# Performance work log

Hardware: AMD Instinct MI355X
Metric: run time of the kernel (lower is better)

The kernel has to match this reference:

```python
import jax, jax.numpy as jnp
import numpy as np

BSZ, IN_DIM, HID, OUT_DIM, N_ITERS = 262144, 64, 128, 64, 30


def setup_inputs() -> dict:
    key = jax.random.key(0)
    ks = jax.random.split(key, 6)
    s_h = 1.0 / np.sqrt(HID)
    s_i = 1.0 / np.sqrt(IN_DIM)
    return {
        "x": jax.random.normal(ks[0], (BSZ, IN_DIM), dtype=jnp.float32),
        "Wz": jax.random.uniform(ks[1], (HID, HID), jnp.float32, -s_h, s_h) * 0.9,  # scaled for contraction
        "Ux": jax.random.uniform(ks[2], (HID, IN_DIM), jnp.float32, -s_i, s_i),
        "b": jax.random.uniform(ks[3], (HID,), jnp.float32, -s_h, s_h),
        "Wd": jax.random.uniform(ks[4], (OUT_DIM, HID), jnp.float32, -s_h, s_h),
        "bd": jax.random.uniform(ks[5], (OUT_DIM,), jnp.float32, -s_h, s_h),
        "n_iters": N_ITERS,
    }


def reference(x, Wz, Ux, b, Wd, bd, n_iters):
    # injection term is iteration-invariant: compute once
    inj = x @ Ux.T + b                     # [B, HID]
    z0 = jnp.zeros((x.shape[0], Wz.shape[0]), dtype=x.dtype)

    def step(z, _):
        z = jax.nn.relu(z @ Wz.T + inj)    # f(z, x)
        return z, None

    z_star, _ = jax.lax.scan(step, z0, None, length=n_iters)
    return z_star @ Wd.T + bd              # decoder Linear
```

## Files before the change

### kernel.cpp

```cpp
#include <hip/hip_runtime.h>


typedef __attribute__((ext_vector_type(8))) __bf16 bf16x8;
typedef __attribute__((ext_vector_type(4))) __bf16 bf16x4;
typedef __attribute__((ext_vector_type(4))) float  floatx4;

#define MFMA16(a, b, c) __builtin_amdgcn_mfma_f32_16x16x32_bf16((a), (b), (c), 0, 0, 0)

static constexpr int kBsz = 262144;
static constexpr int kTM  = 32;

__device__ __forceinline__ bf16x8 cvt_bf16x8(float4 a, float4 b) {
  bf16x8 r;
  r[0] = (__bf16)a.x; r[1] = (__bf16)a.y; r[2] = (__bf16)a.z; r[3] = (__bf16)a.w;
  r[4] = (__bf16)b.x; r[5] = (__bf16)b.y; r[6] = (__bf16)b.z; r[7] = (__bf16)b.w;
  return r;
}

__global__ void __launch_bounds__(256, 4) deq_fused(
    const float* __restrict__ x,
    const float* __restrict__ Wz,
    const float* __restrict__ Ux,
    const float* __restrict__ bvec,
    const float* __restrict__ Wd,
    const float* __restrict__ bd,
    const int*  __restrict__ n_iters_p,
    float* __restrict__ out)
{
  __shared__ __align__(16) __bf16 zl[2][kTM][136];

  const int tid  = threadIdx.x;
  const int lane = tid & 63;
  const int wv   = tid >> 6;
  const int wn   = wv & 1;
  const int wm   = wv >> 1;
  const int l15  = lane & 15;
  const int quad = lane >> 4;
  const int row0 = blockIdx.x * kTM;
  const int ml   = 16 * wm + l15;
  const int iters = *n_iters_p;

  bf16x8 awz[4][4];
#pragma unroll
  for (int nt = 0; nt < 4; ++nt) {
    const int n = 64 * wn + 16 * nt + l15;
#pragma unroll
    for (int ks = 0; ks < 4; ++ks) {
      const float4* p = (const float4*)(Wz + n * 128 + 32 * ks + 8 * quad);
      awz[nt][ks] = cvt_bf16x8(p[0], p[1]);
    }
  }

  floatx4 inj[4];
#pragma unroll
  for (int nt = 0; nt < 4; ++nt) {
    const float4 bv = *(const float4*)(bvec + 64 * wn + 16 * nt + 4 * quad);
    floatx4 v = {bv.x, bv.y, bv.z, bv.w};
    inj[nt] = v;
  }
  {
    bf16x8 bx[2];
#pragma unroll
    for (int ks = 0; ks < 2; ++ks) {
      const float4* p = (const float4*)(x + (size_t)(row0 + ml) * 64 + 32 * ks + 8 * quad);
      bx[ks] = cvt_bf16x8(p[0], p[1]);
    }
#pragma unroll
    for (int nt = 0; nt < 4; ++nt) {
      const int n = 64 * wn + 16 * nt + l15;
#pragma unroll
      for (int ks = 0; ks < 2; ++ks) {
        const float4* p = (const float4*)(Ux + n * 64 + 32 * ks + 8 * quad);
        const bf16x8 a = cvt_bf16x8(p[0], p[1]);
        inj[nt] = MFMA16(a, bx[ks], inj[nt]);
      }
    }
  }

#pragma unroll
  for (int nt = 0; nt < 4; ++nt) {
    bf16x4 z4;
#pragma unroll
    for (int i = 0; i < 4; ++i) z4[i] = (__bf16)fmaxf(inj[nt][i], 0.0f);
    *(bf16x4*)&zl[0][ml][64 * wn + 16 * nt + 4 * quad] = z4;
  }

  int pb = 0;
  for (int t = 0; t < iters - 1; ++t) {
    __syncthreads();
    bf16x8 bz[4];
#pragma unroll
    for (int ks = 0; ks < 4; ++ks)
      bz[ks] = *(const bf16x8*)&zl[pb][ml][32 * ks + 8 * quad];
    const int nb = pb ^ 1;
#pragma unroll
    for (int nt = 0; nt < 4; ++nt) {
      floatx4 acc = inj[nt];
#pragma unroll
      for (int ks = 0; ks < 4; ++ks)
        acc = MFMA16(awz[nt][ks], bz[ks], acc);
      bf16x4 z4;
#pragma unroll
      for (int i = 0; i < 4; ++i) z4[i] = (__bf16)fmaxf(acc[i], 0.0f);
      *(bf16x4*)&zl[nb][ml][64 * wn + 16 * nt + 4 * quad] = z4;
    }
    pb = nb;
  }
  __syncthreads();

  bf16x8 awd[2][4];
#pragma unroll
  for (int ot = 0; ot < 2; ++ot) {
    const int o = 32 * wn + 16 * ot + l15;
#pragma unroll
    for (int ks = 0; ks < 4; ++ks) {
      const float4* p = (const float4*)(Wd + o * 128 + 32 * ks + 8 * quad);
      awd[ot][ks] = cvt_bf16x8(p[0], p[1]);
    }
  }
  {
    bf16x8 bz[4];
#pragma unroll
    for (int ks = 0; ks < 4; ++ks)
      bz[ks] = *(const bf16x8*)&zl[pb][ml][32 * ks + 8 * quad];
#pragma unroll
    for (int ot = 0; ot < 2; ++ot) {
      const float4 bv = *(const float4*)(bd + 32 * wn + 16 * ot + 4 * quad);
      floatx4 acc = {bv.x, bv.y, bv.z, bv.w};
#pragma unroll
      for (int ks = 0; ks < 4; ++ks)
        acc = MFMA16(awd[ot][ks], bz[ks], acc);
      float4 ov;
      ov.x = acc[0]; ov.y = acc[1]; ov.z = acc[2]; ov.w = acc[3];
      *(float4*)(out + (size_t)(row0 + ml) * 64 + 32 * wn + 16 * ot + 4 * quad) = ov;
    }
  }
}

extern "C" void kernel_launch(void* const* d_in, const int* in_sizes, int n_in,
                              void* d_out, int out_size, void* d_ws, size_t ws_size,
                              hipStream_t stream) {
  const float* x  = (const float*)d_in[0];
  const float* Wz = (const float*)d_in[1];
  const float* Ux = (const float*)d_in[2];
  const float* b  = (const float*)d_in[3];
  const float* Wd = (const float*)d_in[4];
  const float* bd = (const float*)d_in[5];
  const int* n_it = (const int*)d_in[6];
  float* outp = (float*)d_out;
  (void)in_sizes; (void)n_in; (void)d_ws; (void)ws_size; (void)out_size;

  dim3 grid(kBsz / kTM);
  deq_fused<<<grid, 256, 0, stream>>>(x, Wz, Ux, b, Wd, bd, n_it, outp);
}
```

Baseline: 378.9 us.

## Split decoder into separate kernel, staging bf16 fixed point in output buffer

Splits the fused kernel in two. The iteration kernel now writes the final bf16 z tile into the output buffer as scratch, and a second kernel reads it back, applies the Wd decoder with MFMA and overwrites the same rows with fp32 results. The intent is to free the decoder weight registers and code from the long iteration loop, which may lower register pressure or raise occupancy. In exchange it adds a second launch and roughly 128 MB of extra global memory traffic, and it relies on each row being read before it is overwritten in place.

```diff
diff --git a/kernel.cpp b/kernel.cpp
--- a/kernel.cpp
+++ b/kernel.cpp
@@ -9,6 +9,7 @@
 
 static constexpr int kBsz = 262144;
 static constexpr int kTM  = 32;
+static constexpr int kLd  = 136;
 
 __device__ __forceinline__ bf16x8 cvt_bf16x8(float4 a, float4 b) {
   bf16x8 r;
@@ -17,17 +18,15 @@
   return r;
 }
 
-__global__ void __launch_bounds__(256, 4) deq_fused(
+__global__ void __launch_bounds__(256, 4) deq_loop(
     const float* __restrict__ x,
     const float* __restrict__ Wz,
     const float* __restrict__ Ux,
     const float* __restrict__ bvec,
-    const float* __restrict__ Wd,
-    const float* __restrict__ bd,
     const int*  __restrict__ n_iters_p,
-    float* __restrict__ out)
+    __bf16* __restrict__ zout)
 {
-  __shared__ __align__(16) __bf16 zl[2][kTM][136];
+  __shared__ __align__(16) __bf16 zl[2][kTM][kLd];
 
   const int tid  = threadIdx.x;
   const int lane = tid & 63;
@@ -108,32 +107,46 @@
   }
   __syncthreads();
 
-  bf16x8 awd[2][4];
+  const int r = tid >> 3;
+  const int c = (tid & 7) * 16;
+  const bf16x8 zlo = *(const bf16x8*)&zl[pb][r][c];
+  const bf16x8 zhi = *(const bf16x8*)&zl[pb][r][c + 8];
+  *(bf16x8*)&zout[(size_t)(row0 + r) * 128 + c] = zlo;
+  *(bf16x8*)&zout[(size_t)(row0 + r) * 128 + c + 8] = zhi;
+}
+
+__global__ void __launch_bounds__(256) deq_dec(
+    const float* __restrict__ Wd,
+    const float* __restrict__ bd,
+    float* __restrict__ out)
+{
+  const int tid  = threadIdx.x;
+  const int lane = tid & 63;
+  const int wv   = tid >> 6;
+  const int l15  = lane & 15;
+  const int quad = lane >> 4;
+  const int row  = blockIdx.x * 64 + 16 * wv + l15;
+  const __bf16* zin = (const __bf16*)out;
+
+  bf16x8 bz[4];
 #pragma unroll
-  for (int ot = 0; ot < 2; ++ot) {
-    const int o = 32 * wn + 16 * ot + l15;
+  for (int ks = 0; ks < 4; ++ks)
+    bz[ks] = *(const bf16x8*)&zin[(size_t)row * 128 + 32 * ks + 8 * quad];
+
+#pragma unroll
+  for (int ot = 0; ot < 4; ++ot) {
+    const int o = 16 * ot + l15;
+    const float4 bv = *(const float4*)(bd + 16 * ot + 4 * quad);
+    floatx4 acc = {bv.x, bv.y, bv.z, bv.w};
 #pragma unroll
     for (int ks = 0; ks < 4; ++ks) {
       const float4* p = (const float4*)(Wd + o * 128 + 32 * ks + 8 * quad);
-      awd[ot][ks] = cvt_bf16x8(p[0], p[1]);
+      const bf16x8 a = cvt_bf16x8(p[0], p[1]);
+      acc = MFMA16(a, bz[ks], acc);
     }
-  }
-  {
-    bf16x8 bz[4];
-#pragma unroll
-    for (int ks = 0; ks < 4; ++ks)
-      bz[ks] = *(const bf16x8*)&zl[pb][ml][32 * ks + 8 * quad];
-#pragma unroll
-    for (int ot = 0; ot < 2; ++ot) {
-      const float4 bv = *(const float4*)(bd + 32 * wn + 16 * ot + 4 * quad);
-      floatx4 acc = {bv.x, bv.y, bv.z, bv.w};
-#pragma unroll
-      for (int ks = 0; ks < 4; ++ks)
-        acc = MFMA16(awd[ot][ks], bz[ks], acc);
-      float4 ov;
-      ov.x = acc[0]; ov.y = acc[1]; ov.z = acc[2]; ov.w = acc[3];
-      *(float4*)(out + (size_t)(row0 + ml) * 64 + 32 * wn + 16 * ot + 4 * quad) = ov;
-    }
+    float4 ov;
+    ov.x = acc[0]; ov.y = acc[1]; ov.z = acc[2]; ov.w = acc[3];
+    *(float4*)(out + (size_t)row * 64 + 16 * ot + 4 * quad) = ov;
   }
 }
 
@@ -150,6 +163,8 @@
   float* outp = (float*)d_out;
   (void)in_sizes; (void)n_in; (void)d_ws; (void)ws_size; (void)out_size;
 
-  dim3 grid(kBsz / kTM);
-  deq_fused<<<grid, 256, 0, stream>>>(x, Wz, Ux, b, Wd, bd, n_it, outp);
+  dim3 g1(kBsz / kTM);
+  deq_loop<<<g1, 256, 0, stream>>>(x, Wz, Ux, b, n_it, (__bf16*)outp);
+  dim3 g2(kBsz / 64);
+  deq_dec<<<g2, 256, 0, stream>>>(Wd, bd, outp);
 }
```

After: 390.9 us. 1.03x slower.

## Pack injection term to bf16 registers and interleave MFMA chains across tiles

Applied to the files above, without the earlier changes.

Stores the iteration-invariant injection term as packed bf16 pairs (8 registers instead of 16 floats) and unpacks it into the accumulators each iteration, lowering register pressure. The inner loop now issues the MFMAs k-step outer and n-tile inner, so the four accumulator chains are independent and LDS loads are split into two halves. Precomputed LDS offsets are used, and decoder weights are converted on the fly rather than held in registers. The cost is a small precision loss on the injection term plus extra unpack ALU work per iteration. A stray dead LDS read expression is also left in.

```diff
diff --git a/kernel.cpp b/kernel.cpp
--- a/kernel.cpp
+++ b/kernel.cpp
@@ -3,18 +3,27 @@
 
 typedef __attribute__((ext_vector_type(8))) __bf16 bf16x8;
 typedef __attribute__((ext_vector_type(4))) __bf16 bf16x4;
+typedef __attribute__((ext_vector_type(2))) __bf16 bf16x2;
 typedef __attribute__((ext_vector_type(4))) float  floatx4;
 
 #define MFMA16(a, b, c) __builtin_amdgcn_mfma_f32_16x16x32_bf16((a), (b), (c), 0, 0, 0)
 
 static constexpr int kBsz = 262144;
 static constexpr int kTM  = 32;
+static constexpr int kLd  = 136;
 
 __device__ __forceinline__ bf16x8 cvt_bf16x8(float4 a, float4 b) {
   bf16x8 r;
   r[0] = (__bf16)a.x; r[1] = (__bf16)a.y; r[2] = (__bf16)a.z; r[3] = (__bf16)a.w;
   r[4] = (__bf16)b.x; r[5] = (__bf16)b.y; r[6] = (__bf16)b.z; r[7] = (__bf16)b.w;
   return r;
+}
+
+__device__ __forceinline__ unsigned pack2(float a, float b) {
+  union { bf16x2 h; unsigned u; } x;
+  x.h[0] = (__bf16)a;
+  x.h[1] = (__bf16)b;
+  return x.u;
 }
 
 __global__ void __launch_bounds__(256, 4) deq_fused(
@@ -27,7 +36,7 @@
     const int*  __restrict__ n_iters_p,
     float* __restrict__ out)
 {
-  __shared__ __align__(16) __bf16 zl[2][kTM][136];
+  __shared__ __align__(16) __bf16 zl[2][kTM][kLd];
 
   const int tid  = threadIdx.x;
   const int lane = tid & 63;
@@ -40,6 +49,9 @@
   const int ml   = 16 * wm + l15;
   const int iters = *n_iters_p;
 
+  const int rdo = ml * kLd + 8 * quad;
+  const int wro = ml * kLd + 64 * wn + 4 * quad;
+
   bf16x8 awz[4][4];
 #pragma unroll
   for (int nt = 0; nt < 4; ++nt) {
@@ -51,14 +63,15 @@
     }
   }
 
-  floatx4 inj[4];
+  unsigned injp[8];
+  {
+    floatx4 inj[4];
 #pragma unroll
-  for (int nt = 0; nt < 4; ++nt) {
-    const float4 bv = *(const float4*)(bvec + 64 * wn + 16 * nt + 4 * quad);
-    floatx4 v = {bv.x, bv.y, bv.z, bv.w};
-    inj[nt] = v;
-  }
-  {
+    for (int nt = 0; nt < 4; ++nt) {
+      const float4 bv = *(const float4*)(bvec + 64 * wn + 16 * nt + 4 * quad);
+      floatx4 v = {bv.x, bv.y, bv.z, bv.w};
+      inj[nt] = v;
+    }
     bf16x8 bx[2];
 #pragma unroll
     for (int ks = 0; ks < 2; ++ks) {
@@ -75,65 +88,82 @@
         inj[nt] = MFMA16(a, bx[ks], inj[nt]);
       }
     }
-  }
-
 #pragma unroll
-  for (int nt = 0; nt < 4; ++nt) {
-    bf16x4 z4;
+    for (int nt = 0; nt < 4; ++nt) {
+      bf16x4 z4;
 #pragma unroll
-    for (int i = 0; i < 4; ++i) z4[i] = (__bf16)fmaxf(inj[nt][i], 0.0f);
-    *(bf16x4*)&zl[0][ml][64 * wn + 16 * nt + 4 * quad] = z4;
+      for (int i = 0; i < 4; ++i) z4[i] = (__bf16)fmaxf(inj[nt][i], 0.0f);
+      *(bf16x4*)&zl[0][0][wro + 16 * nt];
+      *(bf16x4*)&zl[0][0][wro + 16 * nt] = z4;
+    }
+#pragma unroll
+    for (int nt = 0; nt < 4; ++nt) {
+      injp[2 * nt]     = pack2(inj[nt][0], inj[nt][1]);
+      injp[2 * nt + 1] = pack2(inj[nt][2], inj[nt][3]);
+    }
   }
 
   int pb = 0;
   for (int t = 0; t < iters - 1; ++t) {
     __syncthreads();
-    bf16x8 bz[4];
-#pragma unroll
-    for (int ks = 0; ks < 4; ++ks)
-      bz[ks] = *(const bf16x8*)&zl[pb][ml][32 * ks + 8 * quad];
-    const int nb = pb ^ 1;
+    const __bf16* src = &zl[pb][0][0];
+    __bf16* dst = &zl[pb ^ 1][0][0];
+    floatx4 acc[4];
 #pragma unroll
     for (int nt = 0; nt < 4; ++nt) {
-      floatx4 acc = inj[nt];
+      const unsigned u0 = injp[2 * nt];
+      const unsigned u1 = injp[2 * nt + 1];
+      acc[nt][0] = __uint_as_float(u0 << 16);
+      acc[nt][1] = __uint_as_float(u0 & 0xffff0000u);
+      acc[nt][2] = __uint_as_float(u1 << 16);
+      acc[nt][3] = __uint_as_float(u1 & 0xffff0000u);
+    }
+    {
+      const bf16x8 b0 = *(const bf16x8*)&src[rdo];
+      const bf16x8 b1 = *(const bf16x8*)&src[rdo + 32];
 #pragma unroll
-      for (int ks = 0; ks < 4; ++ks)
-        acc = MFMA16(awz[nt][ks], bz[ks], acc);
+      for (int nt = 0; nt < 4; ++nt) acc[nt] = MFMA16(awz[nt][0], b0, acc[nt]);
+#pragma unroll
+      for (int nt = 0; nt < 4; ++nt) acc[nt] = MFMA16(awz[nt][1], b1, acc[nt]);
+    }
+    {
+      const bf16x8 b2 = *(const bf16x8*)&src[rdo + 64];
+      const bf16x8 b3 = *(const bf16x8*)&src[rdo + 96];
+#pragma unroll
+      for (int nt = 0; nt < 4; ++nt) acc[nt] = MFMA16(awz[nt][2], b2, acc[nt]);
+#pragma unroll
+      for (int nt = 0; nt < 4; ++nt) acc[nt] = MFMA16(awz[nt][3], b3, acc[nt]);
+    }
+#pragma unroll
+    for (int nt = 0; nt < 4; ++nt) {
       bf16x4 z4;
 #pragma unroll
-      for (int i = 0; i < 4; ++i) z4[i] = (__bf16)fmaxf(acc[i], 0.0f);
-      *(bf16x4*)&zl[nb][ml][64 * wn + 16 * nt + 4 * quad] = z4;
+      for (int i = 0; i < 4; ++i) z4[i] = (__bf16)fmaxf(acc[nt][i], 0.0f);
+      *(bf16x4*)&dst[wro + 16 * nt] = z4;
     }
-    pb = nb;
+    pb ^= 1;
   }
   __syncthreads();
 
-  bf16x8 awd[2][4];
+  const __bf16* zf = &zl[pb][0][0];
+  bf16x8 bz[4];
+#pragma unroll
+  for (int ks = 0; ks < 4; ++ks)
+    bz[ks] = *(const bf16x8*)&zf[rdo + 32 * ks];
 #pragma unroll
   for (int ot = 0; ot < 2; ++ot) {
     const int o = 32 * wn + 16 * ot + l15;
+    const float4 bv = *(const float4*)(bd + 32 * wn + 16 * ot + 4 * quad);
+    floatx4 acc = {bv.x, bv.y, bv.z, bv.w};
 #pragma unroll
     for (int ks = 0; ks < 4; ++ks) {
       const float4* p = (const float4*)(Wd + o * 128 + 32 * ks + 8 * quad);
-      awd[ot][ks] = cvt_bf16x8(p[0], p[1]);
+      const bf16x8 a = cvt_bf16x8(p[0], p[1]);
+      acc = MFMA16(a, bz[ks], acc);
     }
-  }
-  {
-    bf16x8 bz[4];
-#pragma unroll
-    for (int ks = 0; ks < 4; ++ks)
-      bz[ks] = *(const bf16x8*)&zl[pb][ml][32 * ks + 8 * quad];
-#pragma unroll
-    for (int ot = 0; ot < 2; ++ot) {
-      const float4 bv = *(const float4*)(bd + 32 * wn + 16 * ot + 4 * quad);
-      floatx4 acc = {bv.x, bv.y, bv.z, bv.w};
-#pragma unroll
-      for (int ks = 0; ks < 4; ++ks)
-        acc = MFMA16(awd[ot][ks], bz[ks], acc);
-      float4 ov;
-      ov.x = acc[0]; ov.y = acc[1]; ov.z = acc[2]; ov.w = acc[3];
-      *(float4*)(out + (size_t)(row0 + ml) * 64 + 32 * wn + 16 * ot + 4 * quad) = ov;
-    }
+    float4 ov;
+    ov.x = acc[0]; ov.y = acc[1]; ov.z = acc[2]; ov.w = acc[3];
+    *(float4*)(out + (size_t)(row0 + ml) * 64 + 32 * wn + 16 * ot + 4 * quad) = ov;
   }
 }
 
```

After: 370.1 us. 2.3% less time.
